# Kernel tuning notes

Measured on AMD Instinct MI355X. Metric: run time of the kernel, lower is better.

The kernel has to match this reference:

```python
import jax, jax.numpy as jnp
import numpy as np

D_MODEL = 1024
NUM_HEADS = 16
D_K = D_MODEL // NUM_HEADS
B, S = 1, 4096


def setup_inputs() -> dict:
    key = jax.random.key(0)
    ks = jax.random.split(key, 11)
    std = 1.0 / np.sqrt(D_MODEL)
    def lin(k):
        kw, kb = jax.random.split(k)
        W = jax.random.uniform(kw, (D_MODEL, D_MODEL), jnp.float32, -std, std)
        b = jax.random.uniform(kb, (D_MODEL,), jnp.float32, -std, std)
        return W, b
    Wq, bq = lin(ks[0]); Wk, bk = lin(ks[1]); Wv, bv = lin(ks[2]); Wo, bo = lin(ks[3])
    q = jax.random.normal(ks[4], (B, S, D_MODEL), jnp.float32)
    k = jax.random.normal(ks[5], (B, S, D_MODEL), jnp.float32)
    v = jax.random.normal(ks[6], (B, S, D_MODEL), jnp.float32)
    return {"q": q, "k": k, "v": v,
            "Wq": Wq, "bq": bq, "Wk": Wk, "bk": bk,
            "Wv": Wv, "bv": bv, "Wo": Wo, "bo": bo}


def reference(q, k, v, Wq, bq, Wk, bk, Wv, bv, Wo, bo):
    Bq, Sq, _ = q.shape
    # Linear projections (torch Linear: x @ W.T + b)
    def split_heads(x):
        return x.reshape(Bq, -1, NUM_HEADS, D_K).transpose(0, 2, 1, 3)  # [B,H,S,Dk]
    query = split_heads(q @ Wq.T + bq)
    key_ = split_heads(k @ Wk.T + bk)
    value = split_heads(v @ Wv.T + bv)
    scores = jnp.einsum('bhsd,bhtd->bhst', query, key_) / jnp.sqrt(jnp.float32(D_K))
    attn = jax.nn.softmax(scores, axis=-1)  # [B,H,S,S]
    ctx = jnp.einsum('bhst,bhtd->bhsd', attn, value)
    ctx = ctx.transpose(0, 2, 1, 3).reshape(Bq, Sq, NUM_HEADS * D_K)
    return ctx @ Wo.T + bo
```

## Files before the change

kernel.cpp:

```cpp
#include <hip/hip_runtime.h>
#include <cstdint>
#include <cstddef>

#define S_LEN 4096
#define DMODEL 1024
#define NHEADS 16
#define DK 64
#define ACT (S_LEN * DMODEL)
#define WELE (DMODEL * DMODEL)

typedef __bf16 bf16;
typedef bf16  bf16x2 __attribute__((ext_vector_type(2)));
typedef bf16  bf16x4 __attribute__((ext_vector_type(4)));
typedef bf16  bf16x8 __attribute__((ext_vector_type(8)));
typedef float f32x4  __attribute__((ext_vector_type(4)));
typedef float f32x16 __attribute__((ext_vector_type(16)));
typedef unsigned int uint32x4v __attribute__((ext_vector_type(4)));

__device__ __forceinline__ void async16(const void* g, void* l) {
    __builtin_amdgcn_global_load_lds(
        (__attribute__((address_space(1))) void*)(uintptr_t)g,
        (__attribute__((address_space(3))) void*)(uintptr_t)l,
        16, 0, 0);
}

__device__ __forceinline__ float fast_exp2(float x) {
#if __has_builtin(__builtin_amdgcn_exp2f)
    return __builtin_amdgcn_exp2f(x);
#else
    return exp2f(x);
#endif
}

__device__ __forceinline__ unsigned pk2(float a, float b) {
    bf16x2 t; t[0] = (bf16)a; t[1] = (bf16)b;
    return __builtin_bit_cast(unsigned, t);
}

__device__ __forceinline__ void pl32swap(unsigned &a, unsigned &b) {
    asm volatile("v_permlane32_swap_b32 %0, %1" : "+v"(a), "+v"(b));
}

__device__ __forceinline__ bf16x8 mkfrag(unsigned w0, unsigned w1, unsigned w2, unsigned w3) {
    uint32x4v u = { w0, w1, w2, w3 };
    return __builtin_bit_cast(bf16x8, u);
}

__global__ void __launch_bounds__(256) cvt7(
    const float* a0, const float* a1, const float* a2,
    const float* w0, const float* w1, const float* w2, const float* w3,
    bf16* oa0, bf16* oa1, bf16* oa2,
    bf16* ow0, bf16* ow1, bf16* ow2, bf16* ow3,
    int nA, int nB)
{
    const float* s; bf16* d; int n4;
    switch (blockIdx.y) {
        case 0: s = a0; d = oa0; n4 = nA; break;
        case 1: s = a1; d = oa1; n4 = nA; break;
        case 2: s = a2; d = oa2; n4 = nA; break;
        case 3: s = w0; d = ow0; n4 = nB; break;
        case 4: s = w1; d = ow1; n4 = nB; break;
        case 5: s = w2; d = ow2; n4 = nB; break;
        default: s = w3; d = ow3; n4 = nB; break;
    }
    int i = blockIdx.x * 256 + threadIdx.x;
    if (i < n4) {
        float4 v = ((const float4*)s)[i];
        bf16x4 r = { (bf16)v.x, (bf16)v.y, (bf16)v.z, (bf16)v.w };
        ((bf16x4*)d)[i] = r;
    }
}

__device__ __forceinline__ void gemm_compute_128(
    const bf16* As, const bf16* Bs, f32x4 (&acc)[4][4],
    int wm, int wn, int l16, int quad)
{
    bf16x8 af[4], bfr[4];
#pragma unroll
    for (int i = 0; i < 4; ++i)
        af[i] = *(const bf16x8*)&As[(wm + i * 16 + l16) * 32 + quad * 8];
#pragma unroll
    for (int i = 0; i < 4; ++i)
        bfr[i] = *(const bf16x8*)&Bs[(wn + i * 16 + l16) * 32 + quad * 8];
#pragma unroll
    for (int mi = 0; mi < 4; ++mi)
#pragma unroll
        for (int ni = 0; ni < 4; ++ni)
            acc[mi][ni] = __builtin_amdgcn_mfma_f32_16x16x32_bf16(
                af[mi], bfr[ni], acc[mi][ni], 0, 0, 0);
}

__device__ __forceinline__ void gemm_core_bk64(
    const bf16* __restrict__ A, const bf16* __restrict__ B,
    bf16* As, bf16* Bs, f32x4 (&acc)[4][4],
    int m0, int n0, int wm, int wn, int K)
{
    const int tid  = threadIdx.x;
    const int wave = tid >> 6;
    const int lane = tid & 63;
    const int quad = lane >> 4;
    const int l16  = lane & 15;

    const int srow = tid >> 2;
    const int scol = (tid & 3) * 8;
    const bf16* Ag = A + (size_t)(m0 + srow) * K + scol;
    const bf16* Bg = B + (size_t)(n0 + srow) * K + scol;
    char* lA = (char*)As + wave * 1024;
    char* lB = (char*)Bs + wave * 1024;

    for (int k0 = 0; k0 < K; k0 += 64) {
        async16(Ag,                       lA);
        async16(Ag + (size_t)64 * K,      lA + 4096);
        async16(Ag + 32,                  lA + 8192);
        async16(Ag + 32 + (size_t)64 * K, lA + 12288);
        async16(Bg,                       lB);
        async16(Bg + (size_t)64 * K,      lB + 4096);
        async16(Bg + 32,                  lB + 8192);
        async16(Bg + 32 + (size_t)64 * K, lB + 12288);
        Ag += 64; Bg += 64;
        __syncthreads();

        gemm_compute_128(As,        Bs,        acc, wm, wn, l16, quad);
        gemm_compute_128(As + 4096, Bs + 4096, acc, wm, wn, l16, quad);
        __syncthreads();
    }
}

__global__ void __launch_bounds__(256) proj_qkv(
    const bf16* __restrict__ Xq, const bf16* __restrict__ Wq, const float* __restrict__ bq, bf16* __restrict__ Qo,
    const bf16* __restrict__ Xk, const bf16* __restrict__ Wk, const float* __restrict__ bk, bf16* __restrict__ Ko,
    const bf16* __restrict__ Xv, const bf16* __restrict__ Wv, const float* __restrict__ bv, bf16* __restrict__ Vo,
    float qscale)
{
    __shared__ __align__(16) bf16 As[2 * 128 * 32];
    __shared__ __align__(16) bf16 Bs[2 * 128 * 32];

    const int which = blockIdx.z;
    const bf16*  A    = (which == 0) ? Xq : (which == 1) ? Xk : Xv;
    const bf16*  Bw   = (which == 0) ? Wq : (which == 1) ? Wk : Wv;
    const float* bias = (which == 0) ? bq : (which == 1) ? bk : bv;
    const float  scale = (which == 0) ? qscale : 1.0f;

    const int tid  = threadIdx.x;
    const int wave = tid >> 6;
    const int lane = tid & 63;
    const int quad = lane >> 4;
    const int l16  = lane & 15;
    const int m0 = blockIdx.x * 128;
    const int n0 = blockIdx.y * 128;
    const int wm = (wave & 1) * 64;
    const int wn = (wave >> 1) * 64;

    f32x4 acc[4][4] = {};
    gemm_core_bk64(A, Bw, As, Bs, acc, m0, n0, wm, wn, DMODEL);

    if (which < 2) {
        bf16* out = (which == 0) ? Qo : Ko;
#pragma unroll
        for (int mi = 0; mi < 4; ++mi)
#pragma unroll
            for (int ni = 0; ni < 4; ++ni) {
                const int n = n0 + wn + ni * 16 + l16;
                const float bn = bias[n];
                const int dk = n & 63;
                const int cc = dk >> 3, ee = dk & 7;
                const size_t hb = (size_t)(n >> 6) * S_LEN * DK;
#pragma unroll
                for (int r = 0; r < 4; ++r) {
                    const int m = m0 + wm + mi * 16 + quad * 4 + r;
                    const int pdk = ((cc ^ (m & 7)) << 3) | ee;
                    out[hb + (size_t)m * DK + pdk] = (bf16)((acc[mi][ni][r] + bn) * scale);
                }
            }
    } else {
#pragma unroll
        for (int mi = 0; mi < 4; ++mi)
#pragma unroll
            for (int ni = 0; ni < 4; ++ni) {
                const int n = n0 + wn + ni * 16 + l16;
                const float bn = bias[n];
                const int dk = n & 63;
                const size_t hb = (size_t)(n >> 6) * (64 * S_LEN);
                const int mbase = m0 + wm + mi * 16 + quad * 4;
                const int T  = mbase >> 6;
                const int tt = mbase & 63;
                const int pos = (((tt >> 3) ^ (dk & 7)) << 3) | (tt & 7);
                bf16x4 r4;
#pragma unroll
                for (int r = 0; r < 4; ++r) r4[r] = (bf16)(acc[mi][ni][r] + bn);
                *(bf16x4*)&Vo[hb + (size_t)T * 4096 + dk * 64 + pos] = r4;
            }
    }
}

__global__ void __launch_bounds__(256) gemm_out(
    const bf16* __restrict__ A, const bf16* __restrict__ Bw,
    const float* __restrict__ bias, float* __restrict__ out)
{
    __shared__ __align__(16) bf16 As[64 * 32];
    __shared__ __align__(16) bf16 Bs[128 * 32];

    const int tid  = threadIdx.x;
    const int wave = tid >> 6;
    const int lane = tid & 63;
    const int quad = lane >> 4;
    const int l16  = lane & 15;
    const int m0 = blockIdx.x * 64;
    const int n0 = blockIdx.y * 128;
    const int wm = (wave & 1) * 32;
    const int wn = (wave >> 1) * 64;

    const int srow = tid >> 2;
    const int scol = (tid & 3) * 8;
    const bf16* Ag  = A  + (size_t)(m0 + srow) * DMODEL + scol;
    const bf16* Bg  = Bw + (size_t)(n0 + srow) * DMODEL + scol;
    const bf16* Bg2 = Bg + (size_t)64 * DMODEL;

    f32x4 acc[2][4] = {};
    for (int k0 = 0; k0 < DMODEL; k0 += 32) {
        async16(Ag,  (char*)As + wave * 1024);
        async16(Bg,  (char*)Bs + wave * 1024);
        async16(Bg2, (char*)Bs + 4096 + wave * 1024);
        Ag += 32; Bg += 32; Bg2 += 32;
        __syncthreads();

        bf16x8 af[2], bfr[4];
#pragma unroll
        for (int i = 0; i < 2; ++i)
            af[i] = *(const bf16x8*)&As[(wm + i * 16 + l16) * 32 + quad * 8];
#pragma unroll
        for (int i = 0; i < 4; ++i)
            bfr[i] = *(const bf16x8*)&Bs[(wn + i * 16 + l16) * 32 + quad * 8];

#pragma unroll
        for (int mi = 0; mi < 2; ++mi)
#pragma unroll
            for (int ni = 0; ni < 4; ++ni)
                acc[mi][ni] = __builtin_amdgcn_mfma_f32_16x16x32_bf16(
                    af[mi], bfr[ni], acc[mi][ni], 0, 0, 0);
        __syncthreads();
    }

#pragma unroll
    for (int mi = 0; mi < 2; ++mi)
#pragma unroll
        for (int ni = 0; ni < 4; ++ni) {
            const int n = n0 + wn + ni * 16 + l16;
            const float bn = bias[n];
#pragma unroll
            for (int r = 0; r < 4; ++r) {
                const int m = m0 + wm + mi * 16 + quad * 4 + r;
                out[(size_t)m * DMODEL + n] = acc[mi][ni][r] + bn;
            }
        }
}

__global__ void __launch_bounds__(512) flash_attn(
    const bf16* __restrict__ Q, const bf16* __restrict__ Kh,
    const bf16* __restrict__ Vt, bf16* __restrict__ ctx)
{
    __shared__ __align__(16) bf16 Qs[256 * 64];
    __shared__ __align__(16) bf16 Ks[2][64 * 64];
    __shared__ __align__(16) bf16 Vs[2][64 * 64];

    const int tid  = threadIdx.x;
    const int wave = tid >> 6;
    const int lane = tid & 63;
    const int l31  = lane & 31;
    const int hi   = lane >> 5;
    const int x7   = lane & 7;
    const int s0 = blockIdx.x * 256;
    const int h  = blockIdx.y;

    const bf16* Kg = Kh + (size_t)h * S_LEN * DK + tid * 8;
    const bf16* Vg = Vt + (size_t)h * (64 * S_LEN) + tid * 8;

    {
        const bf16* Qg = Q + (size_t)h * S_LEN * DK + (size_t)s0 * DK + tid * 8;
#pragma unroll
        for (int j = 0; j < 4; ++j)
            async16(Qg + j * 4096, (char*)Qs + j * 8192 + wave * 1024);
    }
    async16(Kg, (char*)Ks + wave * 1024);
    async16(Vg, (char*)Vs + wave * 1024);
    Kg += 4096; Vg += 4096;
    __syncthreads();

    bf16x8 qf[4];
    {
        const bf16* qb = &Qs[(wave * 32 + l31) * 64];
#pragma unroll
        for (int ks = 0; ks < 4; ++ks)
            qf[ks] = *(const bf16x8*)(qb + ((((ks << 1) + hi) ^ x7) << 3));
    }

    f32x16 od[2] = {};
    float lsum = 0.0f;
    int cur = 0;

    for (int it = 0; it < 64; ++it) {
        if (it < 63) {
            async16(Kg, (char*)Ks + (cur ^ 1) * 8192 + wave * 1024);
            async16(Vg, (char*)Vs + (cur ^ 1) * 8192 + wave * 1024);
            Kg += 4096; Vg += 4096;
        }
        const bf16* Kc = &Ks[cur][0];
        const bf16* Vc = &Vs[cur][0];

        f32x16 st[2] = {};
        __builtin_amdgcn_s_setprio(1);
#pragma unroll
        for (int tt = 0; tt < 2; ++tt) {
            const bf16* kb = &Kc[(tt * 32 + l31) * 64];
#pragma unroll
            for (int ks = 0; ks < 4; ++ks) {
                bf16x8 kf = *(const bf16x8*)(kb + ((((ks << 1) + hi) ^ x7) << 3));
                st[tt] = __builtin_amdgcn_mfma_f32_32x32x16_bf16(kf, qf[ks], st[tt], 0, 0, 0);
            }
        }
        __builtin_amdgcn_s_setprio(0);

        bf16x8 pf[4];
#pragma unroll
        for (int tt = 0; tt < 2; ++tt) {
            float p[16];
#pragma unroll
            for (int r = 0; r < 16; ++r) {
                p[r] = fast_exp2(st[tt][r]);
                lsum += p[r];
            }
#pragma unroll
            for (int w = 0; w < 2; ++w) {
                const int G = w * 8;
                unsigned A0 = pk2(p[G + 0], p[G + 1]);
                unsigned A1 = pk2(p[G + 2], p[G + 3]);
                unsigned B0 = pk2(p[G + 4], p[G + 5]);
                unsigned B1 = pk2(p[G + 6], p[G + 7]);
                pl32swap(A0, B0);
                pl32swap(A1, B1);
                pf[tt * 2 + w] = mkfrag(A0, A1, B0, B1);
            }
        }

        __builtin_amdgcn_s_setprio(1);
#pragma unroll
        for (int dd = 0; dd < 2; ++dd) {
            const bf16* vb = &Vc[(dd * 32 + l31) * 64];
#pragma unroll
            for (int ks = 0; ks < 4; ++ks) {
                bf16x8 vf = *(const bf16x8*)(vb + ((((ks << 1) + hi) ^ x7) << 3));
                od[dd] = __builtin_amdgcn_mfma_f32_32x32x16_bf16(vf, pf[ks], od[dd], 0, 0, 0);
            }
        }
        __builtin_amdgcn_s_setprio(0);

        __syncthreads();
        cur ^= 1;
    }

    lsum += __shfl_xor(lsum, 32);
    const float rinv = 1.0f / lsum;
    const int s = s0 + wave * 32 + l31;
#pragma unroll
    for (int dd = 0; dd < 2; ++dd)
#pragma unroll
        for (int g = 0; g < 4; ++g) {
            bf16x4 r4;
#pragma unroll
            for (int r = 0; r < 4; ++r)
                r4[r] = (bf16)(od[dd][g * 4 + r] * rinv);
            *(bf16x4*)&ctx[(size_t)s * DMODEL + h * DK + dd * 32 + g * 8 + hi * 4] = r4;
        }
}

extern "C" void kernel_launch(void* const* d_in, const int* in_sizes, int n_in,
                              void* d_out, int out_size, void* d_ws, size_t ws_size,
                              hipStream_t stream)
{
    (void)in_sizes; (void)n_in; (void)out_size; (void)ws_size;
    const float* q  = (const float*)d_in[0];
    const float* k  = (const float*)d_in[1];
    const float* v  = (const float*)d_in[2];
    const float* Wq = (const float*)d_in[3];
    const float* bq = (const float*)d_in[4];
    const float* Wk = (const float*)d_in[5];
    const float* bk = (const float*)d_in[6];
    const float* Wv = (const float*)d_in[7];
    const float* bv = (const float*)d_in[8];
    const float* Wo = (const float*)d_in[9];
    const float* bo = (const float*)d_in[10];

    bf16* Xq  = (bf16*)d_ws;
    bf16* Xk  = Xq  + ACT;
    bf16* Xv  = Xk  + ACT;
    bf16* Wqb = Xv  + ACT;
    bf16* Wkb = Wqb + WELE;
    bf16* Wvb = Wkb + WELE;
    bf16* Wob = Wvb + WELE;
    bf16* Qh  = Wob + WELE;
    bf16* Kh  = Qh  + ACT;
    bf16* Vt  = Kh  + ACT;
    bf16* CTX = Vt  + ACT;

    cvt7<<<dim3(ACT / 4 / 256, 7), 256, 0, stream>>>(
        q, k, v, Wq, Wk, Wv, Wo,
        Xq, Xk, Xv, Wqb, Wkb, Wvb, Wob, ACT / 4, WELE / 4);

    const float qscale = 0.125f * 1.4426950408889634f;
    proj_qkv<<<dim3(S_LEN / 128, DMODEL / 128, 3), 256, 0, stream>>>(
        Xq, Wqb, bq, Qh, Xk, Wkb, bk, Kh, Xv, Wvb, bv, Vt, qscale);

    flash_attn<<<dim3(S_LEN / 256, NHEADS), 512, 0, stream>>>(Qh, Kh, Vt, CTX);

    gemm_out<<<dim3(S_LEN / 64, DMODEL / 128), 256, 0, stream>>>(CTX, Wob, bo, (float*)d_out);
}
```

Measured before the change: 252.7 us.

## Triple-buffer K/V tiles in flash attention with partial vmcnt waits

```diff
diff --git a/kernel.cpp b/kernel.cpp
--- a/kernel.cpp
+++ b/kernel.cpp
@@ -260,8 +260,8 @@
     const bf16* __restrict__ Vt, bf16* __restrict__ ctx)
 {
     __shared__ __align__(16) bf16 Qs[256 * 64];
-    __shared__ __align__(16) bf16 Ks[2][64 * 64];
-    __shared__ __align__(16) bf16 Vs[2][64 * 64];
+    __shared__ __align__(16) bf16 Ks[3][64 * 64];
+    __shared__ __align__(16) bf16 Vs[3][64 * 64];
 
     const int tid  = threadIdx.x;
     const int wave = tid >> 6;
@@ -284,7 +284,12 @@
     async16(Kg, (char*)Ks + wave * 1024);
     async16(Vg, (char*)Vs + wave * 1024);
     Kg += 4096; Vg += 4096;
-    __syncthreads();
+    async16(Kg, (char*)Ks + 8192 + wave * 1024);
+    async16(Vg, (char*)Vs + 8192 + wave * 1024);
+    Kg += 4096; Vg += 4096;
+    asm volatile("s_waitcnt vmcnt(2)" ::: "memory");
+    __builtin_amdgcn_s_barrier();
+    __builtin_amdgcn_sched_barrier(0);
 
     bf16x8 qf[4];
     {
@@ -296,16 +301,10 @@
 
     f32x16 od[2] = {};
     float lsum = 0.0f;
-    int cur = 0;
-
-    for (int it = 0; it < 64; ++it) {
-        if (it < 63) {
-            async16(Kg, (char*)Ks + (cur ^ 1) * 8192 + wave * 1024);
-            async16(Vg, (char*)Vs + (cur ^ 1) * 8192 + wave * 1024);
-            Kg += 4096; Vg += 4096;
-        }
-        const bf16* Kc = &Ks[cur][0];
-        const bf16* Vc = &Vs[cur][0];
+
+    auto compute = [&](int cb) {
+        const bf16* Kc = &Ks[cb][0];
+        const bf16* Vc = &Vs[cb][0];
 
         f32x16 st[2] = {};
         __builtin_amdgcn_s_setprio(1);
@@ -353,10 +352,28 @@
             }
         }
         __builtin_amdgcn_s_setprio(0);
-
-        __syncthreads();
-        cur ^= 1;
-    }
+    };
+
+    int cur = 0;
+    for (int it = 0; it < 62; ++it) {
+        int nb = cur + 2; if (nb >= 3) nb -= 3;
+        async16(Kg, (char*)Ks + nb * 8192 + wave * 1024);
+        async16(Vg, (char*)Vs + nb * 8192 + wave * 1024);
+        Kg += 4096; Vg += 4096;
+
+        compute(cur);
+
+        asm volatile("s_waitcnt vmcnt(2)" ::: "memory");
+        __builtin_amdgcn_s_barrier();
+        __builtin_amdgcn_sched_barrier(0);
+        cur = (cur + 1 == 3) ? 0 : cur + 1;
+    }
+    compute(cur);
+    asm volatile("s_waitcnt vmcnt(0)" ::: "memory");
+    __builtin_amdgcn_s_barrier();
+    __builtin_amdgcn_sched_barrier(0);
+    cur = (cur + 1 == 3) ? 0 : cur + 1;
+    compute(cur);
 
     lsum += __shfl_xor(lsum, 32);
     const float rinv = 1.0f / lsum;
```

After: 254.9 us. No clear change (+0.8%).

## Split attention KV range in two and combine partial outputs

Applied to the files above, without the earlier changes.

```diff
diff --git a/kernel.cpp b/kernel.cpp
--- a/kernel.cpp
+++ b/kernel.cpp
@@ -257,7 +257,9 @@
 
 __global__ void __launch_bounds__(512) flash_attn(
     const bf16* __restrict__ Q, const bf16* __restrict__ Kh,
-    const bf16* __restrict__ Vt, bf16* __restrict__ ctx)
+    const bf16* __restrict__ Vt,
+    float* __restrict__ O0, float* __restrict__ O1lo, float* __restrict__ O1hi,
+    float* __restrict__ lsums)
 {
     __shared__ __align__(16) bf16 Qs[256 * 64];
     __shared__ __align__(16) bf16 Ks[2][64 * 64];
@@ -271,9 +273,10 @@
     const int x7   = lane & 7;
     const int s0 = blockIdx.x * 256;
     const int h  = blockIdx.y;
-
-    const bf16* Kg = Kh + (size_t)h * S_LEN * DK + tid * 8;
-    const bf16* Vg = Vt + (size_t)h * (64 * S_LEN) + tid * 8;
+    const int z  = blockIdx.z;
+
+    const bf16* Kg = Kh + (size_t)h * S_LEN * DK + (size_t)z * 2048 * DK + tid * 8;
+    const bf16* Vg = Vt + (size_t)h * (64 * S_LEN) + (size_t)z * 32 * 4096 + tid * 8;
 
     {
         const bf16* Qg = Q + (size_t)h * S_LEN * DK + (size_t)s0 * DK + tid * 8;
@@ -298,8 +301,8 @@
     float lsum = 0.0f;
     int cur = 0;
 
-    for (int it = 0; it < 64; ++it) {
-        if (it < 63) {
+    for (int it = 0; it < 32; ++it) {
+        if (it < 31) {
             async16(Kg, (char*)Ks + (cur ^ 1) * 8192 + wave * 1024);
             async16(Vg, (char*)Vs + (cur ^ 1) * 8192 + wave * 1024);
             Kg += 4096; Vg += 4096;
@@ -358,19 +361,39 @@
         cur ^= 1;
     }
 
-    lsum += __shfl_xor(lsum, 32);
-    const float rinv = 1.0f / lsum;
+    float* Ob = (z == 0) ? O0
+              : (s0 < 2048 ? O1lo : O1hi - (size_t)2048 * DMODEL);
+    float* lz = lsums + (size_t)z * S_LEN * NHEADS;
+
+    float ls = lsum + __shfl_xor(lsum, 32);
     const int s = s0 + wave * 32 + l31;
+    if (hi == 0) lz[s * NHEADS + h] = ls;
+    float* bp = Ob + (size_t)s * DMODEL + h * DK;
 #pragma unroll
     for (int dd = 0; dd < 2; ++dd)
 #pragma unroll
         for (int g = 0; g < 4; ++g) {
-            bf16x4 r4;
-#pragma unroll
-            for (int r = 0; r < 4; ++r)
-                r4[r] = (bf16)(od[dd][g * 4 + r] * rinv);
-            *(bf16x4*)&ctx[(size_t)s * DMODEL + h * DK + dd * 32 + g * 8 + hi * 4] = r4;
-        }
+            f32x4 r4 = { od[dd][g * 4 + 0], od[dd][g * 4 + 1],
+                         od[dd][g * 4 + 2], od[dd][g * 4 + 3] };
+            *(f32x4*)&bp[dd * 32 + g * 8 + hi * 4] = r4;
+        }
+}
+
+__global__ void __launch_bounds__(256) combine(
+    const float* __restrict__ O0, const float* __restrict__ O1lo,
+    const float* __restrict__ O1hi, const float* __restrict__ lsums,
+    bf16* __restrict__ ctxn)
+{
+    const int idx = blockIdx.x * 256 + threadIdx.x;
+    const int s = idx >> 8;
+    float4 a = ((const float4*)O0)[idx];
+    float4 b = (s < 2048) ? ((const float4*)O1lo)[idx]
+                          : ((const float4*)O1hi)[idx - 2048 * 256];
+    const int sh = idx >> 4;
+    const float rinv = 1.0f / (lsums[sh] + lsums[S_LEN * NHEADS + sh]);
+    bf16x4 r = { (bf16)((a.x + b.x) * rinv), (bf16)((a.y + b.y) * rinv),
+                 (bf16)((a.z + b.z) * rinv), (bf16)((a.w + b.w) * rinv) };
+    ((bf16x4*)ctxn)[idx] = r;
 }
 
 extern "C" void kernel_launch(void* const* d_in, const int* in_sizes, int n_in,
@@ -402,6 +425,12 @@
     bf16* Vt  = Kh  + ACT;
     bf16* CTX = Vt  + ACT;
 
+    float* O0    = (float*)Xq;
+    float* O1lo  = (float*)CTX;
+    float* O1hi  = (float*)Xv;
+    float* lsums = (float*)Wkb;
+    bf16*  CTXn  = Qh;
+
     cvt7<<<dim3(ACT / 4 / 256, 7), 256, 0, stream>>>(
         q, k, v, Wq, Wk, Wv, Wo,
         Xq, Xk, Xv, Wqb, Wkb, Wvb, Wob, ACT / 4, WELE / 4);
@@ -410,7 +439,10 @@
     proj_qkv<<<dim3(S_LEN / 128, DMODEL / 128, 3), 256, 0, stream>>>(
         Xq, Wqb, bq, Qh, Xk, Wkb, bk, Kh, Xv, Wvb, bv, Vt, qscale);
 
-    flash_attn<<<dim3(S_LEN / 256, NHEADS), 512, 0, stream>>>(Qh, Kh, Vt, CTX);
-
-    gemm_out<<<dim3(S_LEN / 64, DMODEL / 128), 256, 0, stream>>>(CTX, Wob, bo, (float*)d_out);
-}
+    flash_attn<<<dim3(S_LEN / 256, NHEADS, 2), 512, 0, stream>>>(
+        Qh, Kh, Vt, O0, O1lo, O1hi, lsums);
+
+    combine<<<dim3(ACT / 4 / 256), 256, 0, stream>>>(O0, O1lo, O1hi, lsums, CTXn);
+
+    gemm_out<<<dim3(S_LEN / 64, DMODEL / 128), 256, 0, stream>>>(CTXn, Wob, bo, (float*)d_out);
+}
```

Result: slower. 258.9 us (+2.4%).
